# Optimization experiments

Measured on AMD Instinct MI355X. Metric: run time of the kernel, lower is better.

## Reference

```python
import jax, jax.numpy as jnp
import numpy as np

B, T, C, H = 2, 2048, 1024, 16
D = C // H  # head dim = 64

def setup_inputs() -> dict:
    key = jax.random.key(0)
    ks = jax.random.split(key, 6)
    s = 0.02
    return {
        "x":  jax.random.normal(ks[0], (B, T, C), dtype=jnp.float32),
        "Wk": jax.random.normal(ks[1], (C, C), dtype=jnp.float32) * s,
        "Wq": jax.random.normal(ks[2], (C, C), dtype=jnp.float32) * s,
        "Wv": jax.random.normal(ks[3], (C, C), dtype=jnp.float32) * s,
        "Wp": jax.random.normal(ks[4], (C, C), dtype=jnp.float32) * s,
        "bp": jax.random.normal(ks[5], (C,), dtype=jnp.float32) * s,
    }

def reference(x, Wk, Wq, Wv, Wp, bp):
    Bs, Ts, Cs = x.shape
    # torch Linear: y = x @ W.T  (W is [out, in])
    def proj_heads(W):
        p = jnp.einsum('btc,dc->btd', x, W)
        return p.reshape(Bs, Ts, H, D).transpose(0, 2, 1, 3)  # [B,H,T,D]
    k = proj_heads(Wk)
    q = proj_heads(Wq)
    v = proj_heads(Wv)
    scale = 1.0 / jnp.sqrt(jnp.asarray(D, dtype=x.dtype))
    att = jnp.einsum('bhtd,bhsd->bhts', q, k) * scale  # [B,H,T,T]
    att = jax.nn.softmax(att, axis=-1)  # NOTE: no causal mask in the original forward
    y = jnp.einsum('bhts,bhsd->bhtd', att, v)
    y = y.transpose(0, 2, 1, 3).reshape(Bs, Ts, Cs)
    return jnp.einsum('btc,dc->btd', y, Wp) + bp
```

## Files before the change

kernel.cpp:

```cpp
#include <hip/hip_runtime.h>
#include <hip/hip_bf16.h>


typedef __bf16 bf16x8 __attribute__((ext_vector_type(8)));
typedef __bf16 bf16x4 __attribute__((ext_vector_type(4)));
typedef float  f32x4  __attribute__((ext_vector_type(4)));
typedef unsigned int uint2v __attribute__((ext_vector_type(2)));

#define QSCALE 0.18033688011112042f

__device__ __forceinline__ void gload_lds16(const void* g, void* l) {
  __builtin_amdgcn_global_load_lds((const __attribute__((address_space(1))) void*)g,
                                   (__attribute__((address_space(3))) void*)l, 16, 0, 0);
}
__device__ __forceinline__ unsigned int lds_off(const void* p) {
  return (unsigned int)(uintptr_t)(__attribute__((address_space(3))) const char*)p;
}
template<int IMM>
__device__ __forceinline__ uint2v tr_b64(unsigned int addr) {
  uint2v r;
  asm volatile("ds_read_b64_tr_b16 %0, %1 offset:%2" : "=v"(r) : "v"(addr), "i"(IMM));
  return r;
}

__global__ __launch_bounds__(256) void cvt_bf16(
    const float* __restrict__ x,  const float* __restrict__ wq, const float* __restrict__ wk,
    const float* __restrict__ wv, const float* __restrict__ wp,
    __bf16* __restrict__ xb,  __bf16* __restrict__ wqb, __bf16* __restrict__ wkb,
    __bf16* __restrict__ wvb, __bf16* __restrict__ wpb) {
  long long i = ((long long)blockIdx.x * 256 + threadIdx.x) * 4;
  const float* src; __bf16* dst; long long off;
  if      (i < 4194304LL) { src = x;  dst = xb;  off = i; }
  else if (i < 5242880LL) { src = wq; dst = wqb; off = i - 4194304LL; }
  else if (i < 6291456LL) { src = wk; dst = wkb; off = i - 5242880LL; }
  else if (i < 7340032LL) { src = wv; dst = wvb; off = i - 6291456LL; }
  else                    { src = wp; dst = wpb; off = i - 7340032LL; }
  float4 v = *(const float4*)(src + off);
  bf16x4 o;
  o[0] = (__bf16)v.x; o[1] = (__bf16)v.y; o[2] = (__bf16)v.z; o[3] = (__bf16)v.w;
  *(bf16x4*)(dst + off) = o;
}

__device__ __forceinline__ void gemm_core_128(
    const __bf16* __restrict__ A, const __bf16* __restrict__ Bw,
    int tileM, int tileN, char* smA, char* smB, f32x4 acc[4][4]) {
  const int tid = threadIdx.x;
  const int lane = tid & 63;
  const int wid = tid >> 6;
  const int wr = wid >> 1, wc = wid & 1;
  #pragma unroll 1
  for (int k0 = 0; k0 < 1024; k0 += 64) {
    __syncthreads();
    #pragma unroll
    for (int r = 0; r < 4; ++r) {
      int ci = tid + 256 * r;
      int row = ci >> 3, c = ci & 7;
      int sc = (c ^ (row & 7)) * 8;
      gload_lds16(A  + (long long)(tileM + row) * 1024 + k0 + sc, smA + ci * 16);
      gload_lds16(Bw + (long long)(tileN + row) * 1024 + k0 + sc, smB + ci * 16);
    }
    __syncthreads();
    #pragma unroll
    for (int kk = 0; kk < 2; ++kk) {
      bf16x8 af[4], bfr[4];
      #pragma unroll
      for (int i = 0; i < 4; ++i) {
        int mrow = wr * 64 + i * 16 + (lane & 15);
        af[i]  = *(const bf16x8*)(smA + mrow * 128 +
                   ((kk * 64 + (lane >> 4) * 16) ^ ((mrow & 7) << 4)));
        int nrow = wc * 64 + i * 16 + (lane & 15);
        bfr[i] = *(const bf16x8*)(smB + nrow * 128 +
                   ((kk * 64 + (lane >> 4) * 16) ^ ((nrow & 7) << 4)));
      }
      __builtin_amdgcn_s_setprio(1);
      #pragma unroll
      for (int mi = 0; mi < 4; ++mi)
        #pragma unroll
        for (int ni = 0; ni < 4; ++ni)
          acc[mi][ni] = __builtin_amdgcn_mfma_f32_16x16x32_bf16(af[mi], bfr[ni], acc[mi][ni], 0, 0, 0);
      __builtin_amdgcn_s_setprio(0);
    }
  }
}

__global__ __launch_bounds__(256) void gemm_qkv(
    const __bf16* __restrict__ Xb, const __bf16* __restrict__ Wqb,
    const __bf16* __restrict__ Wkb, const __bf16* __restrict__ Wvb,
    __bf16* __restrict__ Qh, __bf16* __restrict__ Kh, __bf16* __restrict__ Vh) {
  __shared__ __align__(16) char smA[16384];
  __shared__ __align__(16) char smB[16384];
  const int z = blockIdx.z;
  const __bf16* W = (z == 0) ? Wqb : (z == 1) ? Wkb : Wvb;
  __bf16* dst     = (z == 0) ? Qh  : (z == 1) ? Kh  : Vh;
  const float scale = (z == 0) ? QSCALE : 1.0f;
  const int tileM = blockIdx.x * 128, tileN = blockIdx.y * 128;
  f32x4 acc[4][4] = {};
  gemm_core_128(Xb, W, tileM, tileN, smA, smB, acc);
  const int lane = threadIdx.x & 63, wid = threadIdx.x >> 6;
  const int wr = wid >> 1, wc = wid & 1;
  #pragma unroll
  for (int mi = 0; mi < 4; ++mi) {
    #pragma unroll
    for (int ni = 0; ni < 4; ++ni) {
      int n = tileN + wc * 64 + ni * 16 + (lane & 15);
      int h = n >> 6, d = n & 63;
      #pragma unroll
      for (int r = 0; r < 4; ++r) {
        int m = tileM + wr * 64 + mi * 16 + (lane >> 4) * 4 + r;
        int b = m >> 11, t = m & 2047;
        dst[((b * 16 + h) * 2048 + t) * 64 + d] = (__bf16)(acc[mi][ni][r] * scale);
      }
    }
  }
}

__global__ __launch_bounds__(256) void gemm_proj(
    const __bf16* __restrict__ Yb, const __bf16* __restrict__ Wpb,
    const float* __restrict__ bias, float* __restrict__ out) {
  __shared__ __align__(16) char smA[16384];
  __shared__ __align__(16) char smB[16384];
  const int tileM = blockIdx.x * 128, tileN = blockIdx.y * 128;
  f32x4 acc[4][4] = {};
  gemm_core_128(Yb, Wpb, tileM, tileN, smA, smB, acc);
  const int lane = threadIdx.x & 63, wid = threadIdx.x >> 6;
  const int wr = wid >> 1, wc = wid & 1;
  #pragma unroll
  for (int mi = 0; mi < 4; ++mi) {
    #pragma unroll
    for (int ni = 0; ni < 4; ++ni) {
      int n = tileN + wc * 64 + ni * 16 + (lane & 15);
      float bv = bias[n];
      #pragma unroll
      for (int r = 0; r < 4; ++r) {
        int m = tileM + wr * 64 + mi * 16 + (lane >> 4) * 4 + r;
        out[(long long)m * 1024 + n] = acc[mi][ni][r] + bv;
      }
    }
  }
}

template<int KS>
__device__ __forceinline__ void pv_half(unsigned int trP, unsigned int trV,
                                        f32x4 Oa[2][4], f32x4 Osum[2], bf16x8 ones) {
  uint2v pl[2], ph[2];
  pl[0] = tr_b64<0 * 2048 + KS * 1024      >(trP);
  ph[0] = tr_b64<0 * 2048 + KS * 1024 + 512>(trP);
  pl[1] = tr_b64<1 * 2048 + KS * 1024      >(trP);
  ph[1] = tr_b64<1 * 2048 + KS * 1024 + 512>(trP);
  uint2v t0[4], t1[4];
  t0[0] = tr_b64<KS * 1024 + 0 * 2048>(trV);  t1[0] = tr_b64<KS * 1024 + 0 * 2048 + 512>(trV);
  t0[1] = tr_b64<KS * 1024 + 1 * 2048>(trV);  t1[1] = tr_b64<KS * 1024 + 1 * 2048 + 512>(trV);
  t0[2] = tr_b64<KS * 1024 + 2 * 2048>(trV);  t1[2] = tr_b64<KS * 1024 + 2 * 2048 + 512>(trV);
  t0[3] = tr_b64<KS * 1024 + 3 * 2048>(trV);  t1[3] = tr_b64<KS * 1024 + 3 * 2048 + 512>(trV);
  asm volatile("s_waitcnt lgkmcnt(0)");
  __builtin_amdgcn_sched_barrier(0);
  __builtin_amdgcn_s_setprio(1);
  bf16x8 pa[2];
  #pragma unroll
  for (int mi = 0; mi < 2; ++mi) {
    uint4 u; u.x = pl[mi][0]; u.y = pl[mi][1]; u.z = ph[mi][0]; u.w = ph[mi][1];
    pa[mi] = __builtin_bit_cast(bf16x8, u);
    Osum[mi] = __builtin_amdgcn_mfma_f32_16x16x32_bf16(pa[mi], ones, Osum[mi], 0, 0, 0);
  }
  #pragma unroll
  for (int nd = 0; nd < 4; ++nd) {
    uint4 u; u.x = t0[nd][0]; u.y = t0[nd][1]; u.z = t1[nd][0]; u.w = t1[nd][1];
    bf16x8 vf = __builtin_bit_cast(bf16x8, u);
    #pragma unroll
    for (int mi = 0; mi < 2; ++mi)
      Oa[mi][nd] = __builtin_amdgcn_mfma_f32_16x16x32_bf16(pa[mi], vf, Oa[mi][nd], 0, 0, 0);
  }
  __builtin_amdgcn_s_setprio(0);
}

__global__ __launch_bounds__(256) void attn(
    const __bf16* __restrict__ Qh, const __bf16* __restrict__ Kh,
    const __bf16* __restrict__ Vh, float* __restrict__ Opart,
    float* __restrict__ lpart) {
  __shared__ __align__(16) char Ksm[2][8192];
  __shared__ __align__(16) char Vsm[2][8192];
  __shared__ __align__(16) char Psm[16384];
  const int tid = threadIdx.x, lane = tid & 63, wid = tid >> 6;
  const int bh = blockIdx.x;
  const int qb = blockIdx.y;
  const int split = blockIdx.z;
  const int base = bh * (2048 * 64);
  const int qrow0 = qb * 128 + wid * 32;
  const int key0 = split * 1024;

  bf16x8 qf[2][2];
  #pragma unroll
  for (int mi = 0; mi < 2; ++mi)
    #pragma unroll
    for (int kk = 0; kk < 2; ++kk)
      qf[mi][kk] = *(const bf16x8*)(Qh + base + (qrow0 + mi * 16 + (lane & 15)) * 64
                                    + kk * 32 + (lane >> 4) * 8);

  bf16x8 ones;
  #pragma unroll
  for (int j = 0; j < 8; ++j) ones[j] = (__bf16)1.0f;

  f32x4 Oa[2][4] = {};
  f32x4 Osum[2] = {};
  char* Pw = Psm + wid * 4096;
  const unsigned int trP = lds_off(Psm) + wid * 4096 + lane * 8;

  int ksrc[2], kdst[2], vsrc[2], vdst[2];
  #pragma unroll
  for (int r = 0; r < 2; ++r) {
    int ci = tid + 256 * r;
    int row = ci >> 3, c = ci & 7;
    int sc = (c ^ (row & 7)) * 8;
    ksrc[r] = base + (key0 + row) * 64 + sc;
    kdst[r] = ci * 16;
    int cc = wid + 4 * r;
    int ks = cc & 1, d4 = cc >> 1;
    int key = ks * 32 + ((lane >> 3) & 3) * 8 + ((lane >> 5) & 1) * 4 + ((lane >> 1) & 3);
    int d = d4 * 16 + (lane & 1) * 8;
    vsrc[r] = base + (key0 + key) * 64 + d;
    vdst[r] = ks * 1024 + d4 * 2048 + lane * 16;
  }

  #pragma unroll
  for (int r = 0; r < 2; ++r) {
    gload_lds16(Kh + ksrc[r], &Ksm[0][0] + kdst[r]);
    gload_lds16(Vh + vsrc[r], &Vsm[0][0] + vdst[r]);
  }
  __syncthreads();
  int buf = 0;

  #pragma unroll 1
  for (int kt = 0; kt < 16; ++kt) {
    if (kt < 15) {
      #pragma unroll
      for (int r = 0; r < 2; ++r) {
        gload_lds16(Kh + ksrc[r] + (kt + 1) * 4096, &Ksm[buf ^ 1][0] + kdst[r]);
        gload_lds16(Vh + vsrc[r] + (kt + 1) * 4096, &Vsm[buf ^ 1][0] + vdst[r]);
      }
    }
    __builtin_amdgcn_sched_barrier(0);

    const char* Kb = &Ksm[buf][0];
    const unsigned int trV = lds_off(Vsm) + buf * 8192 + lane * 8;

    f32x4 S[2][4] = {};
    #pragma unroll
    for (int kk = 0; kk < 2; ++kk) {
      bf16x8 kf[4];
      #pragma unroll
      for (int ni = 0; ni < 4; ++ni) {
        int row = ni * 16 + (lane & 15);
        kf[ni] = *(const bf16x8*)(Kb + row * 128 +
                   ((kk * 64 + (lane >> 4) * 16) ^ ((row & 7) << 4)));
      }
      __builtin_amdgcn_s_setprio(1);
      #pragma unroll
      for (int mi = 0; mi < 2; ++mi)
        #pragma unroll
        for (int ni = 0; ni < 4; ++ni)
          S[mi][ni] = __builtin_amdgcn_mfma_f32_16x16x32_bf16(qf[mi][kk], kf[ni], S[mi][ni], 0, 0, 0);
      __builtin_amdgcn_s_setprio(0);
    }

    #pragma unroll
    for (int mi = 0; mi < 2; ++mi) {
      #pragma unroll
      for (int ni = 0; ni < 4; ++ni) {
        bf16x4 pb;
        #pragma unroll
        for (int r = 0; r < 4; ++r) pb[r] = (__bf16)exp2f(fminf(S[mi][ni][r], 60.0f));
        int kq = ni * 16 + (lane & 15);
        *(bf16x4*)(Pw + mi * 2048 + (kq >> 5) * 1024 + ((kq >> 2) & 1) * 512 +
                   ((kq >> 3) & 3) * 128 + (kq & 3) * 32 + (lane >> 4) * 8) = pb;
      }
    }

    pv_half<0>(trP, trV, Oa, Osum, ones);
    pv_half<1>(trP, trV, Oa, Osum, ones);

    __syncthreads();
    buf ^= 1;
  }

  float* Op = Opart + (long long)(split * 32 + bh) * 2048 * 64;
  float* lp = lpart + (split * 32 + bh) * 2048;
  #pragma unroll
  for (int mi = 0; mi < 2; ++mi) {
    #pragma unroll
    for (int r = 0; r < 4; ++r) {
      int t = qrow0 + mi * 16 + (lane >> 4) * 4 + r;
      if ((lane & 15) == 0) lp[t] = Osum[mi][r];
      #pragma unroll
      for (int nd = 0; nd < 4; ++nd)
        Op[(long long)t * 64 + nd * 16 + (lane & 15)] = Oa[mi][nd][r];
    }
  }
}

__global__ __launch_bounds__(256) void attn_combine(
    const float* __restrict__ Opart, const float* __restrict__ lpart,
    __bf16* __restrict__ Yb) {
  int i = blockIdx.x * 256 + threadIdx.x;
  int row = i >> 4;
  int d0 = (i & 15) * 4;
  float4 o0 = *(const float4*)(Opart + (long long)row * 64 + d0);
  float4 o1 = *(const float4*)(Opart + 4194304LL + (long long)row * 64 + d0);
  float inv = 1.0f / (lpart[row] + lpart[65536 + row]);
  int bh = row >> 11, t = row & 2047;
  int b = bh >> 4, h = bh & 15;
  bf16x4 o;
  o[0] = (__bf16)((o0.x + o1.x) * inv); o[1] = (__bf16)((o0.y + o1.y) * inv);
  o[2] = (__bf16)((o0.z + o1.z) * inv); o[3] = (__bf16)((o0.w + o1.w) * inv);
  *(bf16x4*)(Yb + ((long long)(b * 2048 + t)) * 1024 + h * 64 + d0) = o;
}

extern "C" void kernel_launch(void* const* d_in, const int* in_sizes, int n_in,
                              void* d_out, int out_size, void* d_ws, size_t ws_size,
                              hipStream_t stream) {
  const float* x  = (const float*)d_in[0];
  const float* Wk = (const float*)d_in[1];
  const float* Wq = (const float*)d_in[2];
  const float* Wv = (const float*)d_in[3];
  const float* Wp = (const float*)d_in[4];
  const float* bp = (const float*)d_in[5];
  float* out = (float*)d_out;

  char* ws = (char*)d_ws;
  __bf16* Xb  = (__bf16*)ws;
  __bf16* Wqb = Xb  + 4194304;
  __bf16* Wkb = Wqb + 1048576;
  __bf16* Wvb = Wkb + 1048576;
  __bf16* Wpb = Wvb + 1048576;
  __bf16* Qh  = Wpb + 1048576;
  __bf16* Kh  = Qh  + 4194304;
  __bf16* Vh  = Kh  + 4194304;
  __bf16* Yb  = Vh  + 4194304;
  float*  Opart = (float*)(Yb + 4194304);
  float*  lpart = Opart + 8388608;

  cvt_bf16<<<8192, 256, 0, stream>>>(x, Wq, Wk, Wv, Wp, Xb, Wqb, Wkb, Wvb, Wpb);
  gemm_qkv<<<dim3(32, 8, 3), 256, 0, stream>>>(Xb, Wqb, Wkb, Wvb, Qh, Kh, Vh);
  attn<<<dim3(32, 16, 2), 256, 0, stream>>>(Qh, Kh, Vh, Opart, lpart);
  attn_combine<<<4096, 256, 0, stream>>>(Opart, lpart, Yb);
  gemm_proj<<<dim3(32, 8), 256, 0, stream>>>(Yb, Wpb, bp, out);
}
```

Measured before the change: 208.5 us.

## Widen attention blocks to 512 threads, shrink proj GEMM M-tile, precompute LDS offsets

The attention kernel now uses 512-thread blocks covering 256 query rows. Each block loads a K/V tile once and shares it across 8 waves, halving global K/V traffic per query. LDS addresses for K fragments and P stores are precomputed outside the loop, and the exp2 clamp is dropped. The output projection GEMM is templated to a 64-row M tile, doubling its grid to 512 blocks for better CU occupancy. Removing the clamp risks overflow if scores exceed the bf16/float range, and the larger attention block needs more LDS per block.

```diff
diff --git a/kernel.cpp b/kernel.cpp
--- a/kernel.cpp
+++ b/kernel.cpp
@@ -41,9 +41,10 @@
   *(bf16x4*)(dst + off) = o;
 }
 
-__device__ __forceinline__ void gemm_core_128(
+template<int MFR>
+__device__ __forceinline__ void gemm_core(
     const __bf16* __restrict__ A, const __bf16* __restrict__ Bw,
-    int tileM, int tileN, char* smA, char* smB, f32x4 acc[4][4]) {
+    int tileM, int tileN, char* smA, char* smB, f32x4 (&acc)[MFR][4]) {
   const int tid = threadIdx.x;
   const int lane = tid & 63;
   const int wid = tid >> 6;
@@ -52,29 +53,38 @@
   for (int k0 = 0; k0 < 1024; k0 += 64) {
     __syncthreads();
     #pragma unroll
+    for (int r = 0; r < MFR; ++r) {
+      int ci = tid + 256 * r;
+      int row = ci >> 3, c = ci & 7;
+      int sc = (c ^ (row & 7)) * 8;
+      gload_lds16(A + (long long)(tileM + row) * 1024 + k0 + sc, smA + ci * 16);
+    }
+    #pragma unroll
     for (int r = 0; r < 4; ++r) {
       int ci = tid + 256 * r;
       int row = ci >> 3, c = ci & 7;
       int sc = (c ^ (row & 7)) * 8;
-      gload_lds16(A  + (long long)(tileM + row) * 1024 + k0 + sc, smA + ci * 16);
       gload_lds16(Bw + (long long)(tileN + row) * 1024 + k0 + sc, smB + ci * 16);
     }
     __syncthreads();
     #pragma unroll
     for (int kk = 0; kk < 2; ++kk) {
-      bf16x8 af[4], bfr[4];
+      bf16x8 af[MFR], bfr[4];
+      #pragma unroll
+      for (int i = 0; i < MFR; ++i) {
+        int mrow = wr * (MFR * 16) + i * 16 + (lane & 15);
+        af[i] = *(const bf16x8*)(smA + mrow * 128 +
+                  ((kk * 64 + (lane >> 4) * 16) ^ ((mrow & 7) << 4)));
+      }
       #pragma unroll
       for (int i = 0; i < 4; ++i) {
-        int mrow = wr * 64 + i * 16 + (lane & 15);
-        af[i]  = *(const bf16x8*)(smA + mrow * 128 +
-                   ((kk * 64 + (lane >> 4) * 16) ^ ((mrow & 7) << 4)));
         int nrow = wc * 64 + i * 16 + (lane & 15);
         bfr[i] = *(const bf16x8*)(smB + nrow * 128 +
-                   ((kk * 64 + (lane >> 4) * 16) ^ ((nrow & 7) << 4)));
+                  ((kk * 64 + (lane >> 4) * 16) ^ ((nrow & 7) << 4)));
       }
       __builtin_amdgcn_s_setprio(1);
       #pragma unroll
-      for (int mi = 0; mi < 4; ++mi)
+      for (int mi = 0; mi < MFR; ++mi)
         #pragma unroll
         for (int ni = 0; ni < 4; ++ni)
           acc[mi][ni] = __builtin_amdgcn_mfma_f32_16x16x32_bf16(af[mi], bfr[ni], acc[mi][ni], 0, 0, 0);
@@ -95,7 +105,7 @@
   const float scale = (z == 0) ? QSCALE : 1.0f;
   const int tileM = blockIdx.x * 128, tileN = blockIdx.y * 128;
   f32x4 acc[4][4] = {};
-  gemm_core_128(Xb, W, tileM, tileN, smA, smB, acc);
+  gemm_core<4>(Xb, W, tileM, tileN, smA, smB, acc);
   const int lane = threadIdx.x & 63, wid = threadIdx.x >> 6;
   const int wr = wid >> 1, wc = wid & 1;
   #pragma unroll
@@ -117,22 +127,22 @@
 __global__ __launch_bounds__(256) void gemm_proj(
     const __bf16* __restrict__ Yb, const __bf16* __restrict__ Wpb,
     const float* __restrict__ bias, float* __restrict__ out) {
-  __shared__ __align__(16) char smA[16384];
+  __shared__ __align__(16) char smA[8192];
   __shared__ __align__(16) char smB[16384];
-  const int tileM = blockIdx.x * 128, tileN = blockIdx.y * 128;
-  f32x4 acc[4][4] = {};
-  gemm_core_128(Yb, Wpb, tileM, tileN, smA, smB, acc);
+  const int tileM = blockIdx.x * 64, tileN = blockIdx.y * 128;
+  f32x4 acc[2][4] = {};
+  gemm_core<2>(Yb, Wpb, tileM, tileN, smA, smB, acc);
   const int lane = threadIdx.x & 63, wid = threadIdx.x >> 6;
   const int wr = wid >> 1, wc = wid & 1;
   #pragma unroll
-  for (int mi = 0; mi < 4; ++mi) {
+  for (int mi = 0; mi < 2; ++mi) {
     #pragma unroll
     for (int ni = 0; ni < 4; ++ni) {
       int n = tileN + wc * 64 + ni * 16 + (lane & 15);
       float bv = bias[n];
       #pragma unroll
       for (int r = 0; r < 4; ++r) {
-        int m = tileM + wr * 64 + mi * 16 + (lane >> 4) * 4 + r;
+        int m = tileM + wr * 32 + mi * 16 + (lane >> 4) * 4 + r;
         out[(long long)m * 1024 + n] = acc[mi][ni][r] + bv;
       }
     }
@@ -173,19 +183,20 @@
   __builtin_amdgcn_s_setprio(0);
 }
 
-__global__ __launch_bounds__(256) void attn(
+__global__ __launch_bounds__(512, 4) void attn(
     const __bf16* __restrict__ Qh, const __bf16* __restrict__ Kh,
     const __bf16* __restrict__ Vh, float* __restrict__ Opart,
     float* __restrict__ lpart) {
   __shared__ __align__(16) char Ksm[2][8192];
   __shared__ __align__(16) char Vsm[2][8192];
-  __shared__ __align__(16) char Psm[16384];
+  __shared__ __align__(16) char Psm[32768];
   const int tid = threadIdx.x, lane = tid & 63, wid = tid >> 6;
+  const int lo = lane & 15, hi = lane >> 4;
   const int bh = blockIdx.x;
   const int qb = blockIdx.y;
   const int split = blockIdx.z;
   const int base = bh * (2048 * 64);
-  const int qrow0 = qb * 128 + wid * 32;
+  const int qrow0 = qb * 256 + wid * 32;
   const int key0 = split * 1024;
 
   bf16x8 qf[2][2];
@@ -193,8 +204,8 @@
   for (int mi = 0; mi < 2; ++mi)
     #pragma unroll
     for (int kk = 0; kk < 2; ++kk)
-      qf[mi][kk] = *(const bf16x8*)(Qh + base + (qrow0 + mi * 16 + (lane & 15)) * 64
-                                    + kk * 32 + (lane >> 4) * 8);
+      qf[mi][kk] = *(const bf16x8*)(Qh + base + (qrow0 + mi * 16 + lo) * 64
+                                    + kk * 32 + hi * 8);
 
   bf16x8 ones;
   #pragma unroll
@@ -202,41 +213,42 @@
 
   f32x4 Oa[2][4] = {};
   f32x4 Osum[2] = {};
-  char* Pw = Psm + wid * 4096;
   const unsigned int trP = lds_off(Psm) + wid * 4096 + lane * 8;
 
-  int ksrc[2], kdst[2], vsrc[2], vdst[2];
-  #pragma unroll
-  for (int r = 0; r < 2; ++r) {
-    int ci = tid + 256 * r;
-    int row = ci >> 3, c = ci & 7;
-    int sc = (c ^ (row & 7)) * 8;
-    ksrc[r] = base + (key0 + row) * 64 + sc;
-    kdst[r] = ci * 16;
-    int cc = wid + 4 * r;
-    int ks = cc & 1, d4 = cc >> 1;
-    int key = ks * 32 + ((lane >> 3) & 3) * 8 + ((lane >> 5) & 1) * 4 + ((lane >> 1) & 3);
-    int d = d4 * 16 + (lane & 1) * 8;
-    vsrc[r] = base + (key0 + key) * 64 + d;
-    vdst[r] = ks * 1024 + d4 * 2048 + lane * 16;
-  }
-
-  #pragma unroll
-  for (int r = 0; r < 2; ++r) {
-    gload_lds16(Kh + ksrc[r], &Ksm[0][0] + kdst[r]);
-    gload_lds16(Vh + vsrc[r], &Vsm[0][0] + vdst[r]);
-  }
+  unsigned int koff[4];
+  #pragma unroll
+  for (int ni = 0; ni < 4; ++ni) {
+    int row = ni * 16 + lo;
+    koff[ni] = row * 128 + ((hi * 16) ^ ((row & 7) << 4));
+  }
+  unsigned int paddr[2][4];
+  #pragma unroll
+  for (int mi = 0; mi < 2; ++mi)
+    #pragma unroll
+    for (int ni = 0; ni < 4; ++ni) {
+      int kq = ni * 16 + lo;
+      paddr[mi][ni] = wid * 4096 + mi * 2048 + (kq >> 5) * 1024 + ((kq >> 2) & 1) * 512 +
+                      ((kq >> 3) & 3) * 128 + (kq & 3) * 32 + hi * 8;
+    }
+
+  int krow = tid >> 3, kc = tid & 7;
+  int ksrc = base + (key0 + krow) * 64 + (kc ^ (krow & 7)) * 8;
+  int kdst = tid * 16;
+  int vcc = tid >> 6, vks = vcc & 1, vd4 = vcc >> 1;
+  int vkey = vks * 32 + ((lane >> 3) & 3) * 8 + ((lane >> 5) & 1) * 4 + ((lane >> 1) & 3);
+  int vsrc = base + (key0 + vkey) * 64 + vd4 * 16 + (lane & 1) * 8;
+  int vdst = vks * 1024 + vd4 * 2048 + lane * 16;
+
+  gload_lds16(Kh + ksrc, &Ksm[0][0] + kdst);
+  gload_lds16(Vh + vsrc, &Vsm[0][0] + vdst);
   __syncthreads();
   int buf = 0;
 
   #pragma unroll 1
   for (int kt = 0; kt < 16; ++kt) {
     if (kt < 15) {
-      #pragma unroll
-      for (int r = 0; r < 2; ++r) {
-        gload_lds16(Kh + ksrc[r] + (kt + 1) * 4096, &Ksm[buf ^ 1][0] + kdst[r]);
-        gload_lds16(Vh + vsrc[r] + (kt + 1) * 4096, &Vsm[buf ^ 1][0] + vdst[r]);
-      }
+      gload_lds16(Kh + ksrc + (kt + 1) * 4096, &Ksm[buf ^ 1][0] + kdst);
+      gload_lds16(Vh + vsrc + (kt + 1) * 4096, &Vsm[buf ^ 1][0] + vdst);
     }
     __builtin_amdgcn_sched_barrier(0);
 
@@ -248,11 +260,8 @@
     for (int kk = 0; kk < 2; ++kk) {
       bf16x8 kf[4];
       #pragma unroll
-      for (int ni = 0; ni < 4; ++ni) {
-        int row = ni * 16 + (lane & 15);
-        kf[ni] = *(const bf16x8*)(Kb + row * 128 +
-                   ((kk * 64 + (lane >> 4) * 16) ^ ((row & 7) << 4)));
-      }
+      for (int ni = 0; ni < 4; ++ni)
+        kf[ni] = *(const bf16x8*)(Kb + (koff[ni] ^ (kk * 64)));
       __builtin_amdgcn_s_setprio(1);
       #pragma unroll
       for (int mi = 0; mi < 2; ++mi)
@@ -268,10 +277,8 @@
       for (int ni = 0; ni < 4; ++ni) {
         bf16x4 pb;
         #pragma unroll
-        for (int r = 0; r < 4; ++r) pb[r] = (__bf16)exp2f(fminf(S[mi][ni][r], 60.0f));
-        int kq = ni * 16 + (lane & 15);
-        *(bf16x4*)(Pw + mi * 2048 + (kq >> 5) * 1024 + ((kq >> 2) & 1) * 512 +
-                   ((kq >> 3) & 3) * 128 + (kq & 3) * 32 + (lane >> 4) * 8) = pb;
+        for (int r = 0; r < 4; ++r) pb[r] = (__bf16)exp2f(S[mi][ni][r]);
+        *(bf16x4*)(&Psm[0] + paddr[mi][ni]) = pb;
       }
     }
 
@@ -288,11 +295,11 @@
   for (int mi = 0; mi < 2; ++mi) {
     #pragma unroll
     for (int r = 0; r < 4; ++r) {
-      int t = qrow0 + mi * 16 + (lane >> 4) * 4 + r;
-      if ((lane & 15) == 0) lp[t] = Osum[mi][r];
+      int t = qrow0 + mi * 16 + hi * 4 + r;
+      if (lo == 0) lp[t] = Osum[mi][r];
       #pragma unroll
       for (int nd = 0; nd < 4; ++nd)
-        Op[(long long)t * 64 + nd * 16 + (lane & 15)] = Oa[mi][nd][r];
+        Op[(long long)t * 64 + nd * 16 + lo] = Oa[mi][nd][r];
     }
   }
 }
@@ -340,7 +347,7 @@
 
   cvt_bf16<<<8192, 256, 0, stream>>>(x, Wq, Wk, Wv, Wp, Xb, Wqb, Wkb, Wvb, Wpb);
   gemm_qkv<<<dim3(32, 8, 3), 256, 0, stream>>>(Xb, Wqb, Wkb, Wvb, Qh, Kh, Vh);
-  attn<<<dim3(32, 16, 2), 256, 0, stream>>>(Qh, Kh, Vh, Opart, lpart);
+  attn<<<dim3(32, 8, 2), 512, 0, stream>>>(Qh, Kh, Vh, Opart, lpart);
   attn_combine<<<4096, 256, 0, stream>>>(Opart, lpart, Yb);
-  gemm_proj<<<dim3(32, 8), 256, 0, stream>>>(Yb, Wpb, bp, out);
-}
+  gemm_proj<<<dim3(64, 8), 256, 0, stream>>>(Yb, Wpb, bp, out);
+}
```

Result: faster. 189.2 us (-9.2%).
